# Performance work log

Hardware: AMD Instinct MI355X
Metric: run time of the kernel (lower is better)

## Reference

```python
import jax, jax.numpy as jnp
import numpy as np

B, C, D, H, W = 2, 64, 3, 96, 96
CD = C * D  # conv1x1 channel count = in_dim * 3


def setup_inputs() -> dict:
    key = jax.random.key(0)
    ks = jax.random.split(key, 7)
    s = 1.0 / np.sqrt(CD)
    x = jax.random.normal(ks[0], (B, C, D, H, W), dtype=jnp.float32)
    Wq = jax.random.uniform(ks[1], (CD, CD), jnp.float32, -s, s)
    bq = jax.random.uniform(ks[2], (CD,), jnp.float32, -s, s)
    Wk = jax.random.uniform(ks[3], (CD, CD), jnp.float32, -s, s)
    bk = jax.random.uniform(ks[4], (CD,), jnp.float32, -s, s)
    Wv = jax.random.uniform(ks[5], (CD, CD), jnp.float32, -s, s)
    bv = jax.random.uniform(ks[6], (CD,), jnp.float32, -s, s)
    return {"x": x, "Wq": Wq, "bq": bq, "Wk": Wk, "bk": bk, "Wv": Wv, "bv": bv}


def reference(x, Wq, bq, Wk, bk, Wv, bv):
    b, c, d, h, w = x.shape
    n = h * w
    xr = x.reshape(b, c * d, n)  # [B, CD, N]; conv1x1 == channel matmul
    q = jnp.einsum('oc,bcn->bon', Wq, xr) + bq[:, None]  # [B, CD, N]
    k = jnp.einsum('oc,bcn->bon', Wk, xr) + bk[:, None]
    v = jnp.einsum('oc,bcn->bon', Wv, xr) + bv[:, None]
    energy = jnp.einsum('bcn,bcm->bnm', q, k)            # [B, N, N]
    attention = jax.nn.softmax(energy, axis=-1)
    # out = bmm(value, attention^T): out[b,c,m] = sum_n v[b,c,n] * attn[b,m,n]
    out = jnp.einsum('bcn,bmn->bcm', v, attention)       # [B, CD, N]
    return out.reshape(b, c, d, h, w)
```

## Files before the change

### kernel.cpp

```cpp
#include <hip/hip_runtime.h>

#define NSEQ  9216
#define CDIM  192
#define KTILE 64

typedef _Float16 h8_t  __attribute__((ext_vector_type(8)));
typedef _Float16 h4_t  __attribute__((ext_vector_type(4)));
typedef float    f4_t  __attribute__((ext_vector_type(4)));
typedef float    f16v  __attribute__((ext_vector_type(16)));

__global__ __launch_bounds__(256) void wconv_kernel(
    const float* __restrict__ Wq, const float* __restrict__ Wk,
    const float* __restrict__ Wv, _Float16* __restrict__ Wh)
{
    int i = blockIdx.x * 256 + threadIdx.x;
    if (i >= 3 * 9216) return;
    const float* src = (i < 9216) ? Wq : (i < 18432 ? Wk : Wv);
    int r = i % 9216;
    f4_t w = ((const f4_t*)src)[r];
    h4_t h = {(_Float16)w[0], (_Float16)w[1], (_Float16)w[2], (_Float16)w[3]};
    ((h4_t*)Wh)[i] = h;
}

__global__ __launch_bounds__(128) void proj_kernel(
    const float* __restrict__ x, const _Float16* __restrict__ Wh,
    const float* __restrict__ bq, const float* __restrict__ bk,
    const float* __restrict__ bv,
    _Float16* __restrict__ QT, _Float16* __restrict__ KT, _Float16* __restrict__ Vg)
{
    const int tid  = threadIdx.x;
    const int lane = tid & 63, wave = tid >> 6;
    const int L31  = lane & 31, hi = lane >> 5;
    const int idx  = blockIdx.x * 2 + wave;
    const int b    = idx / 288;
    const int n0   = (idx % 288) * 32;
    const int n    = n0 + L31;

    h8_t bf[12];
    #pragma unroll
    for (int t = 0; t < 12; t++) {
        h8_t h;
        #pragma unroll
        for (int j = 0; j < 8; j++)
            h[j] = (_Float16)x[(size_t)(b * CDIM + t * 16 + hi * 8 + j) * NSEQ + n];
        bf[t] = h;
    }

    const float* biases[3] = {bq, bk, bv};
    for (int mat = 0; mat < 3; mat++) {
        const _Float16* W = Wh + mat * CDIM * CDIM;
        f16v acc[6];
        #pragma unroll
        for (int s = 0; s < 6; s++)
            #pragma unroll
            for (int r = 0; r < 16; r++) acc[s][r] = 0.f;

        #pragma unroll
        for (int t = 0; t < 12; t++) {
            #pragma unroll
            for (int s = 0; s < 6; s++) {
                h8_t a = *(const h8_t*)(W + (s * 32 + L31) * CDIM + t * 16 + hi * 8);
                acc[s] = __builtin_amdgcn_mfma_f32_32x32x16_f16(a, bf[t], acc[s], 0, 0, 0);
            }
        }

        if (mat < 2) {
            _Float16* dst = ((mat == 0) ? QT : KT) + ((size_t)b * NSEQ + n) * CDIM;
            #pragma unroll
            for (int s = 0; s < 6; s++) {
                #pragma unroll
                for (int g = 0; g < 4; g++) {
                    f4_t bb = *(const f4_t*)&biases[mat][s * 32 + 8 * g + 4 * hi];
                    h4_t h = {(_Float16)(acc[s][4*g+0] + bb[0]),
                              (_Float16)(acc[s][4*g+1] + bb[1]),
                              (_Float16)(acc[s][4*g+2] + bb[2]),
                              (_Float16)(acc[s][4*g+3] + bb[3])};
                    *(h4_t*)(dst + s * 32 + 8 * g + 4 * hi) = h;
                }
            }
        } else {
            #pragma unroll
            for (int s = 0; s < 6; s++) {
                #pragma unroll
                for (int g = 0; g < 4; g++) {
                    f4_t bb = *(const f4_t*)&biases[2][s * 32 + 8 * g + 4 * hi];
                    #pragma unroll
                    for (int r = 0; r < 4; r++) {
                        int o = s * 32 + 8 * g + 4 * hi + r;
                        Vg[((size_t)b * CDIM + o) * NSEQ + n] =
                            (_Float16)(acc[s][4*g+r] + bb[r]);
                    }
                }
            }
        }
    }
}

template<int NSPLIT>
__global__ __launch_bounds__(256, 2) void flash_kernel(
    const _Float16* __restrict__ QT, const _Float16* __restrict__ KTg,
    const _Float16* __restrict__ Vg,
    _Float16* __restrict__ O_part, float* __restrict__ m_part, float* __restrict__ l_part)
{
    constexpr int KPS    = NSEQ / NSPLIT;
    constexpr int KITERS = KPS / KTILE;

    __shared__ __align__(16) _Float16 K_s[KTILE * 200];
    __shared__ __align__(16) _Float16 V_s[CDIM * 72];
    __shared__ __align__(16) _Float16 P_s[4 * 32 * 72];
    __shared__ float alpha_s[4][32];

    const int tid  = threadIdx.x;
    const int lane = tid & 63, wave = tid >> 6;
    const int L31  = lane & 31, hi = lane >> 5;
    const int qtile = blockIdx.x, split = blockIdx.y, b = blockIdx.z;
    const int q0 = qtile * 128 + wave * 32;

    h8_t qf[12];
    const _Float16* qbase = QT + ((size_t)b * NSEQ + q0 + L31) * CDIM + hi * 8;
    #pragma unroll
    for (int t = 0; t < 12; t++) qf[t] = *(const h8_t*)(qbase + t * 16);

    f16v acc[6];
    #pragma unroll
    for (int s = 0; s < 6; s++)
        #pragma unroll
        for (int r = 0; r < 16; r++) acc[s][r] = 0.f;
    float m_run = -__builtin_inff();
    float l_run = 0.f;

    const _Float16* ksrc = KTg + ((size_t)b * NSEQ + split * KPS) * CDIM;
    const _Float16* vsrc = Vg + (size_t)b * CDIM * NSEQ + split * KPS;

    for (int kt = 0; kt < KITERS; kt++) {
        __syncthreads();
        {
            const h8_t* src = (const h8_t*)(ksrc + (size_t)kt * KTILE * CDIM);
            #pragma unroll
            for (int t = 0; t < 6; t++) {
                int i = tid + t * 256;
                int row = i / 24, col = i % 24;
                *(h8_t*)(K_s + row * 200 + col * 8) = src[i];
            }
            #pragma unroll
            for (int t = 0; t < 6; t++) {
                int i = tid + t * 256;
                int c = i >> 3, seg = i & 7;
                *(h8_t*)(V_s + c * 72 + seg * 8) =
                    *(const h8_t*)(vsrc + (size_t)c * NSEQ + kt * KTILE + seg * 8);
            }
        }
        __syncthreads();

        f16v st[2];
        #pragma unroll
        for (int s = 0; s < 2; s++)
            #pragma unroll
            for (int r = 0; r < 16; r++) st[s][r] = 0.f;
        #pragma unroll
        for (int t = 0; t < 12; t++) {
            #pragma unroll
            for (int s = 0; s < 2; s++) {
                h8_t a = *(const h8_t*)(K_s + (s * 32 + L31) * 200 + t * 16 + hi * 8);
                st[s] = __builtin_amdgcn_mfma_f32_32x32x16_f16(a, qf[t], st[s], 0, 0, 0);
            }
        }

        float mx = st[0][0];
        #pragma unroll
        for (int s = 0; s < 2; s++)
            #pragma unroll
            for (int r = 0; r < 16; r++) mx = fmaxf(mx, st[s][r]);
        mx = fmaxf(mx, __shfl_xor(mx, 32));
        float m_new = fmaxf(m_run, mx);

        float p[32];
        float psum = 0.f;
        #pragma unroll
        for (int s = 0; s < 2; s++)
            #pragma unroll
            for (int r = 0; r < 16; r++) {
                float e = __expf(st[s][r] - m_new);
                p[s * 16 + r] = e;
                psum += e;
            }

        if (__any(m_new > m_run)) {
            float alpha = __expf(m_run - m_new);
            l_run = l_run * alpha + psum;
            if (lane < 32) alpha_s[wave][lane] = alpha;
            __asm__ volatile("" ::: "memory");
            f4_t a4[4];
            #pragma unroll
            for (int g = 0; g < 4; g++)
                a4[g] = *(const f4_t*)&alpha_s[wave][8 * g + 4 * hi];
            #pragma unroll
            for (int cs = 0; cs < 6; cs++)
                #pragma unroll
                for (int r = 0; r < 16; r++) acc[cs][r] *= a4[r >> 2][r & 3];
        } else {
            l_run += psum;
        }
        m_run = m_new;

        _Float16* prow = P_s + wave * 32 * 72 + L31 * 72;
        #pragma unroll
        for (int s = 0; s < 2; s++)
            #pragma unroll
            for (int g = 0; g < 4; g++) {
                h4_t h = {(_Float16)p[s*16+4*g+0], (_Float16)p[s*16+4*g+1],
                          (_Float16)p[s*16+4*g+2], (_Float16)p[s*16+4*g+3]};
                *(h4_t*)(prow + s * 32 + 8 * g + 4 * hi) = h;
            }
        __asm__ volatile("" ::: "memory");

        #pragma unroll
        for (int ks = 0; ks < 4; ks++) {
            h8_t pa = *(const h8_t*)(prow + ks * 16 + hi * 8);
            #pragma unroll
            for (int cs = 0; cs < 6; cs++) {
                h8_t vb = *(const h8_t*)(V_s + (cs * 32 + L31) * 72 + ks * 16 + hi * 8);
                acc[cs] = __builtin_amdgcn_mfma_f32_32x32x16_f16(pa, vb, acc[cs], 0, 0, 0);
            }
        }
    }

    float l_tot = l_run + __shfl_xor(l_run, 32);
    const size_t pbase = (size_t)(b * NSPLIT + split) * NSEQ + q0;
    if (lane < 32) {
        m_part[pbase + lane] = m_run;
        l_part[pbase + lane] = l_tot;
    }
    _Float16* obase = O_part + pbase * CDIM;
    #pragma unroll
    for (int cs = 0; cs < 6; cs++)
        #pragma unroll
        for (int r = 0; r < 16; r++) {
            int q = (r & 3) + 8 * (r >> 2) + 4 * hi;
            obase[(size_t)q * CDIM + cs * 32 + L31] = (_Float16)acc[cs][r];
        }
}

template<int NS>
__global__ __launch_bounds__(256) void combine_kernel(
    const _Float16* __restrict__ O_part, const float* __restrict__ m_part,
    const float* __restrict__ l_part, float* __restrict__ out)
{
    __shared__ float Cs[CDIM][65];
    __shared__ float winv[NS][64];
    const int tid = threadIdx.x;
    const int b  = blockIdx.y;
    const int n0 = blockIdx.x * 64;

    if (tid < 64) {
        int n = n0 + tid;
        float mm[NS], ll[NS], ms = -__builtin_inff();
        #pragma unroll
        for (int s = 0; s < NS; s++) {
            mm[s] = m_part[(b * NS + s) * NSEQ + n];
            ll[s] = l_part[(b * NS + s) * NSEQ + n];
            ms = fmaxf(ms, mm[s]);
        }
        float denom = 0.f;
        #pragma unroll
        for (int s = 0; s < NS; s++) {
            float w = __expf(mm[s] - ms);
            mm[s] = w;
            denom += w * ll[s];
        }
        #pragma unroll
        for (int s = 0; s < NS; s++) winv[s][tid] = mm[s] / denom;
    }
    __syncthreads();

    for (int i = tid; i < 64 * 96; i += 256) {
        int nl = i / 96, cp = i % 96;
        float v0 = 0.f, v1 = 0.f;
        #pragma unroll
        for (int s = 0; s < NS; s++) {
            const _Float16* op =
                O_part + ((size_t)(b * NS + s) * NSEQ + n0 + nl) * CDIM + cp * 2;
            float w = winv[s][nl];
            v0 += w * (float)op[0];
            v1 += w * (float)op[1];
        }
        Cs[cp * 2][nl] = v0;
        Cs[cp * 2 + 1][nl] = v1;
    }
    __syncthreads();
    for (int i = tid; i < CDIM * 64; i += 256) {
        int nl = i & 63, c = i >> 6;
        out[((size_t)b * CDIM + c) * NSEQ + n0 + nl] = Cs[c][nl];
    }
}

extern "C" void kernel_launch(void* const* d_in, const int* in_sizes, int n_in,
                              void* d_out, int out_size, void* d_ws, size_t ws_size,
                              hipStream_t stream)
{
    const float* x  = (const float*)d_in[0];
    const float* Wq = (const float*)d_in[1];
    const float* bq = (const float*)d_in[2];
    const float* Wk = (const float*)d_in[3];
    const float* bk = (const float*)d_in[4];
    const float* Wv = (const float*)d_in[5];
    const float* bv = (const float*)d_in[6];
    float* out = (float*)d_out;

    char* ws = (char*)d_ws;
    _Float16* QT = (_Float16*)(ws);
    _Float16* KT = (_Float16*)(ws + 7077888);
    _Float16* Vg = (_Float16*)(ws + 14155776);
    char* tail = ws + 21233664;
    _Float16* Wh = (_Float16*)tail;
    _Float16* O_part = (_Float16*)tail;

    wconv_kernel<<<108, 256, 0, stream>>>(Wq, Wk, Wv, Wh);
    proj_kernel<<<288, 128, 0, stream>>>(x, Wh, bq, bk, bv, QT, KT, Vg);

    const size_t need8 = 21233664ull + 8 * 7077888ull + 2 * 589824ull;
    const size_t need4 = 21233664ull + 4 * 7077888ull + 2 * 294912ull;
    if (ws_size >= need8) {
        float* m_part = (float*)(tail + 8 * 7077888ull);
        float* l_part = (float*)(tail + 8 * 7077888ull + 589824ull);
        flash_kernel<8><<<dim3(72, 8, 2), 256, 0, stream>>>(QT, KT, Vg, O_part, m_part, l_part);
        combine_kernel<8><<<dim3(144, 2), 256, 0, stream>>>(O_part, m_part, l_part, out);
    } else if (ws_size >= need4) {
        float* m_part = (float*)(tail + 4 * 7077888ull);
        float* l_part = (float*)(tail + 4 * 7077888ull + 294912ull);
        flash_kernel<4><<<dim3(72, 4, 2), 256, 0, stream>>>(QT, KT, Vg, O_part, m_part, l_part);
        combine_kernel<4><<<dim3(144, 2), 256, 0, stream>>>(O_part, m_part, l_part, out);
    } else {
        float* m_part = (float*)(tail + 2 * 7077888ull);
        float* l_part = (float*)(tail + 2 * 7077888ull + 147456ull);
        flash_kernel<2><<<dim3(72, 2, 2), 256, 0, stream>>>(QT, KT, Vg, O_part, m_part, l_part);
        combine_kernel<2><<<dim3(144, 2), 256, 0, stream>>>(O_part, m_part, l_part, out);
    }
}
```

Before: 302.9 us.

## Read K from global, prefetch V in registers, fold log2e into Q, split projection

Several changes at once. The flash kernel drops the K tile from shared memory and reads K straight from global or L2 into MFMA operands. The V tile is prefetched into registers one iteration ahead, which overlaps its load with compute. Q weights and bias are pre-scaled by log2(e) so the softmax can use exp2 directly. The projection kernel now gives each wave one matrix instead of all three, for more parallelism, and the combine kernel uses smaller tiles and vectorized half2 loads. The risk is that uncached global K reads repeated across waves add memory latency, and that the extra prefetch registers reduce occupancy.

```diff
diff --git a/kernel.cpp b/kernel.cpp
--- a/kernel.cpp
+++ b/kernel.cpp
@@ -3,9 +3,11 @@
 #define NSEQ  9216
 #define CDIM  192
 #define KTILE 64
+#define LOG2E 1.44269504088896f
 
 typedef _Float16 h8_t  __attribute__((ext_vector_type(8)));
 typedef _Float16 h4_t  __attribute__((ext_vector_type(4)));
+typedef _Float16 h2_t  __attribute__((ext_vector_type(2)));
 typedef float    f4_t  __attribute__((ext_vector_type(4)));
 typedef float    f16v  __attribute__((ext_vector_type(16)));
 
@@ -16,13 +18,15 @@
     int i = blockIdx.x * 256 + threadIdx.x;
     if (i >= 3 * 9216) return;
     const float* src = (i < 9216) ? Wq : (i < 18432 ? Wk : Wv);
+    float s = (i < 9216) ? LOG2E : 1.f;
     int r = i % 9216;
     f4_t w = ((const f4_t*)src)[r];
-    h4_t h = {(_Float16)w[0], (_Float16)w[1], (_Float16)w[2], (_Float16)w[3]};
+    h4_t h = {(_Float16)(w[0]*s), (_Float16)(w[1]*s),
+              (_Float16)(w[2]*s), (_Float16)(w[3]*s)};
     ((h4_t*)Wh)[i] = h;
 }
 
-__global__ __launch_bounds__(128) void proj_kernel(
+__global__ __launch_bounds__(256) void proj_kernel(
     const float* __restrict__ x, const _Float16* __restrict__ Wh,
     const float* __restrict__ bq, const float* __restrict__ bk,
     const float* __restrict__ bv,
@@ -31,9 +35,11 @@
     const int tid  = threadIdx.x;
     const int lane = tid & 63, wave = tid >> 6;
     const int L31  = lane & 31, hi = lane >> 5;
-    const int idx  = blockIdx.x * 2 + wave;
-    const int b    = idx / 288;
-    const int n0   = (idx % 288) * 32;
+    const int idx  = blockIdx.x * 4 + wave;
+    const int mat  = idx / 576;
+    const int rem  = idx % 576;
+    const int b    = rem / 288;
+    const int n0   = (rem % 288) * 32;
     const int n    = n0 + L31;
 
     h8_t bf[12];
@@ -46,50 +52,50 @@
         bf[t] = h;
     }
 
-    const float* biases[3] = {bq, bk, bv};
-    for (int mat = 0; mat < 3; mat++) {
-        const _Float16* W = Wh + mat * CDIM * CDIM;
-        f16v acc[6];
-        #pragma unroll
-        for (int s = 0; s < 6; s++)
-            #pragma unroll
-            for (int r = 0; r < 16; r++) acc[s][r] = 0.f;
-
-        #pragma unroll
-        for (int t = 0; t < 12; t++) {
-            #pragma unroll
-            for (int s = 0; s < 6; s++) {
-                h8_t a = *(const h8_t*)(W + (s * 32 + L31) * CDIM + t * 16 + hi * 8);
-                acc[s] = __builtin_amdgcn_mfma_f32_32x32x16_f16(a, bf[t], acc[s], 0, 0, 0);
-            }
-        }
-
-        if (mat < 2) {
-            _Float16* dst = ((mat == 0) ? QT : KT) + ((size_t)b * NSEQ + n) * CDIM;
-            #pragma unroll
-            for (int s = 0; s < 6; s++) {
+    const _Float16* W = Wh + mat * CDIM * CDIM;
+    const float* bias = (mat == 0) ? bq : (mat == 1 ? bk : bv);
+    const float bscale = (mat == 0) ? LOG2E : 1.f;
+
+    f16v acc[6];
+    #pragma unroll
+    for (int s = 0; s < 6; s++)
+        #pragma unroll
+        for (int r = 0; r < 16; r++) acc[s][r] = 0.f;
+
+    #pragma unroll
+    for (int t = 0; t < 12; t++) {
+        #pragma unroll
+        for (int s = 0; s < 6; s++) {
+            h8_t a = *(const h8_t*)(W + (s * 32 + L31) * CDIM + t * 16 + hi * 8);
+            acc[s] = __builtin_amdgcn_mfma_f32_32x32x16_f16(a, bf[t], acc[s], 0, 0, 0);
+        }
+    }
+
+    if (mat < 2) {
+        _Float16* dst = ((mat == 0) ? QT : KT) + ((size_t)b * NSEQ + n) * CDIM;
+        #pragma unroll
+        for (int s = 0; s < 6; s++) {
+            #pragma unroll
+            for (int g = 0; g < 4; g++) {
+                f4_t bb = *(const f4_t*)&bias[s * 32 + 8 * g + 4 * hi];
+                h4_t h = {(_Float16)(acc[s][4*g+0] + bb[0] * bscale),
+                          (_Float16)(acc[s][4*g+1] + bb[1] * bscale),
+                          (_Float16)(acc[s][4*g+2] + bb[2] * bscale),
+                          (_Float16)(acc[s][4*g+3] + bb[3] * bscale)};
+                *(h4_t*)(dst + s * 32 + 8 * g + 4 * hi) = h;
+            }
+        }
+    } else {
+        #pragma unroll
+        for (int s = 0; s < 6; s++) {
+            #pragma unroll
+            for (int g = 0; g < 4; g++) {
+                f4_t bb = *(const f4_t*)&bias[s * 32 + 8 * g + 4 * hi];
                 #pragma unroll
-                for (int g = 0; g < 4; g++) {
-                    f4_t bb = *(const f4_t*)&biases[mat][s * 32 + 8 * g + 4 * hi];
-                    h4_t h = {(_Float16)(acc[s][4*g+0] + bb[0]),
-                              (_Float16)(acc[s][4*g+1] + bb[1]),
-                              (_Float16)(acc[s][4*g+2] + bb[2]),
-                              (_Float16)(acc[s][4*g+3] + bb[3])};
-                    *(h4_t*)(dst + s * 32 + 8 * g + 4 * hi) = h;
-                }
-            }
-        } else {
-            #pragma unroll
-            for (int s = 0; s < 6; s++) {
-                #pragma unroll
-                for (int g = 0; g < 4; g++) {
-                    f4_t bb = *(const f4_t*)&biases[2][s * 32 + 8 * g + 4 * hi];
-                    #pragma unroll
-                    for (int r = 0; r < 4; r++) {
-                        int o = s * 32 + 8 * g + 4 * hi + r;
-                        Vg[((size_t)b * CDIM + o) * NSEQ + n] =
-                            (_Float16)(acc[s][4*g+r] + bb[r]);
-                    }
+                for (int r = 0; r < 4; r++) {
+                    int o = s * 32 + 8 * g + 4 * hi + r;
+                    Vg[((size_t)b * CDIM + o) * NSEQ + n] =
+                        (_Float16)(acc[s][4*g+r] + bb[r]);
                 }
             }
         }
@@ -105,7 +111,6 @@
     constexpr int KPS    = NSEQ / NSPLIT;
     constexpr int KITERS = KPS / KTILE;
 
-    __shared__ __align__(16) _Float16 K_s[KTILE * 200];
     __shared__ __align__(16) _Float16 V_s[CDIM * 72];
     __shared__ __align__(16) _Float16 P_s[4 * 32 * 72];
     __shared__ float alpha_s[4][32];
@@ -132,26 +137,32 @@
     const _Float16* ksrc = KTg + ((size_t)b * NSEQ + split * KPS) * CDIM;
     const _Float16* vsrc = Vg + (size_t)b * CDIM * NSEQ + split * KPS;
 
+    const _Float16* vgl[6];
+    _Float16*       vds[6];
+    #pragma unroll
+    for (int t = 0; t < 6; t++) {
+        int i = tid + t * 256;
+        int c = i >> 3, seg = i & 7;
+        vgl[t] = vsrc + (size_t)c * NSEQ + seg * 8;
+        vds[t] = V_s + c * 72 + seg * 8;
+    }
+
+    h8_t vreg[6];
+    #pragma unroll
+    for (int t = 0; t < 6; t++) vreg[t] = *(const h8_t*)(vgl[t]);
+
     for (int kt = 0; kt < KITERS; kt++) {
         __syncthreads();
-        {
-            const h8_t* src = (const h8_t*)(ksrc + (size_t)kt * KTILE * CDIM);
-            #pragma unroll
-            for (int t = 0; t < 6; t++) {
-                int i = tid + t * 256;
-                int row = i / 24, col = i % 24;
-                *(h8_t*)(K_s + row * 200 + col * 8) = src[i];
-            }
-            #pragma unroll
-            for (int t = 0; t < 6; t++) {
-                int i = tid + t * 256;
-                int c = i >> 3, seg = i & 7;
-                *(h8_t*)(V_s + c * 72 + seg * 8) =
-                    *(const h8_t*)(vsrc + (size_t)c * NSEQ + kt * KTILE + seg * 8);
-            }
-        }
+        #pragma unroll
+        for (int t = 0; t < 6; t++) *(h8_t*)(vds[t]) = vreg[t];
         __syncthreads();
-
+        if (kt + 1 < KITERS) {
+            #pragma unroll
+            for (int t = 0; t < 6; t++)
+                vreg[t] = *(const h8_t*)(vgl[t] + (kt + 1) * KTILE);
+        }
+
+        const _Float16* kbase = ksrc + (size_t)kt * KTILE * CDIM;
         f16v st[2];
         #pragma unroll
         for (int s = 0; s < 2; s++)
@@ -161,7 +172,7 @@
         for (int t = 0; t < 12; t++) {
             #pragma unroll
             for (int s = 0; s < 2; s++) {
-                h8_t a = *(const h8_t*)(K_s + (s * 32 + L31) * 200 + t * 16 + hi * 8);
+                h8_t a = *(const h8_t*)(kbase + (s * 32 + L31) * CDIM + t * 16 + hi * 8);
                 st[s] = __builtin_amdgcn_mfma_f32_32x32x16_f16(a, qf[t], st[s], 0, 0, 0);
             }
         }
@@ -180,13 +191,13 @@
         for (int s = 0; s < 2; s++)
             #pragma unroll
             for (int r = 0; r < 16; r++) {
-                float e = __expf(st[s][r] - m_new);
+                float e = __builtin_exp2f(st[s][r] - m_new);
                 p[s * 16 + r] = e;
                 psum += e;
             }
 
         if (__any(m_new > m_run)) {
-            float alpha = __expf(m_run - m_new);
+            float alpha = __builtin_exp2f(m_run - m_new);
             l_run = l_run * alpha + psum;
             if (lane < 32) alpha_s[wave][lane] = alpha;
             __asm__ volatile("" ::: "memory");
@@ -246,13 +257,13 @@
     const _Float16* __restrict__ O_part, const float* __restrict__ m_part,
     const float* __restrict__ l_part, float* __restrict__ out)
 {
-    __shared__ float Cs[CDIM][65];
-    __shared__ float winv[NS][64];
+    __shared__ float Cs[CDIM][33];
+    __shared__ float winv[NS][32];
     const int tid = threadIdx.x;
     const int b  = blockIdx.y;
-    const int n0 = blockIdx.x * 64;
-
-    if (tid < 64) {
+    const int n0 = blockIdx.x * 32;
+
+    if (tid < 32) {
         int n = n0 + tid;
         float mm[NS], ll[NS], ms = -__builtin_inff();
         #pragma unroll
@@ -264,7 +275,7 @@
         float denom = 0.f;
         #pragma unroll
         for (int s = 0; s < NS; s++) {
-            float w = __expf(mm[s] - ms);
+            float w = __builtin_exp2f(mm[s] - ms);
             mm[s] = w;
             denom += w * ll[s];
         }
@@ -273,13 +284,13 @@
     }
     __syncthreads();
 
-    for (int i = tid; i < 64 * 96; i += 256) {
+    for (int i = tid; i < 32 * 96; i += 256) {
         int nl = i / 96, cp = i % 96;
         float v0 = 0.f, v1 = 0.f;
         #pragma unroll
         for (int s = 0; s < NS; s++) {
-            const _Float16* op =
-                O_part + ((size_t)(b * NS + s) * NSEQ + n0 + nl) * CDIM + cp * 2;
+            h2_t op = *(const h2_t*)(O_part +
+                ((size_t)(b * NS + s) * NSEQ + n0 + nl) * CDIM + cp * 2);
             float w = winv[s][nl];
             v0 += w * (float)op[0];
             v1 += w * (float)op[1];
@@ -288,8 +299,8 @@
         Cs[cp * 2 + 1][nl] = v1;
     }
     __syncthreads();
-    for (int i = tid; i < CDIM * 64; i += 256) {
-        int nl = i & 63, c = i >> 6;
+    for (int i = tid; i < CDIM * 32; i += 256) {
+        int nl = i & 31, c = i >> 5;
         out[((size_t)b * CDIM + c) * NSEQ + n0 + nl] = Cs[c][nl];
     }
 }
@@ -316,7 +327,7 @@
     _Float16* O_part = (_Float16*)tail;
 
     wconv_kernel<<<108, 256, 0, stream>>>(Wq, Wk, Wv, Wh);
-    proj_kernel<<<288, 128, 0, stream>>>(x, Wh, bq, bk, bv, QT, KT, Vg);
+    proj_kernel<<<432, 256, 0, stream>>>(x, Wh, bq, bk, bv, QT, KT, Vg);
 
     const size_t need8 = 21233664ull + 8 * 7077888ull + 2 * 589824ull;
     const size_t need4 = 21233664ull + 4 * 7077888ull + 2 * 294912ull;
@@ -324,16 +335,16 @@
         float* m_part = (float*)(tail + 8 * 7077888ull);
         float* l_part = (float*)(tail + 8 * 7077888ull + 589824ull);
         flash_kernel<8><<<dim3(72, 8, 2), 256, 0, stream>>>(QT, KT, Vg, O_part, m_part, l_part);
-        combine_kernel<8><<<dim3(144, 2), 256, 0, stream>>>(O_part, m_part, l_part, out);
+        combine_kernel<8><<<dim3(288, 2), 256, 0, stream>>>(O_part, m_part, l_part, out);
     } else if (ws_size >= need4) {
         float* m_part = (float*)(tail + 4 * 7077888ull);
         float* l_part = (float*)(tail + 4 * 7077888ull + 294912ull);
         flash_kernel<4><<<dim3(72, 4, 2), 256, 0, stream>>>(QT, KT, Vg, O_part, m_part, l_part);
-        combine_kernel<4><<<dim3(144, 2), 256, 0, stream>>>(O_part, m_part, l_part, out);
+        combine_kernel<4><<<dim3(288, 2), 256, 0, stream>>>(O_part, m_part, l_part, out);
     } else {
         float* m_part = (float*)(tail + 2 * 7077888ull);
         float* l_part = (float*)(tail + 2 * 7077888ull + 147456ull);
         flash_kernel<2><<<dim3(72, 2, 2), 256, 0, stream>>>(QT, KT, Vg, O_part, m_part, l_part);
-        combine_kernel<2><<<dim3(144, 2), 256, 0, stream>>>(O_part, m_part, l_part, out);
-    }
-}
+        combine_kernel<2><<<dim3(288, 2), 256, 0, stream>>>(O_part, m_part, l_part, out);
+    }
+}
```

Measured after the change: 417.7 us. +37.9%, slower.

## Split projection across matrices and halves, fold log2e into Q, vectorize combine

Applied to the files above, without the earlier changes.

The projection kernel now gives each wave a single matrix and one half of the output channels, launching six times as many waves to raise parallelism and cut per-wave register pressure. The cost is that x is re-read six times. Wq and bq are pre-scaled by log2(e) so the flash and combine kernels can use exp2 in place of exp, which drops a multiply per exponential. The combine kernel reads four halves per load instead of two, and the row-max reduction is reordered into a shorter tree.

```diff
diff --git a/kernel.cpp b/kernel.cpp
--- a/kernel.cpp
+++ b/kernel.cpp
@@ -3,9 +3,11 @@
 #define NSEQ  9216
 #define CDIM  192
 #define KTILE 64
+#define LOG2E 1.44269504088896f
 
 typedef _Float16 h8_t  __attribute__((ext_vector_type(8)));
 typedef _Float16 h4_t  __attribute__((ext_vector_type(4)));
+typedef _Float16 h2_t  __attribute__((ext_vector_type(2)));
 typedef float    f4_t  __attribute__((ext_vector_type(4)));
 typedef float    f16v  __attribute__((ext_vector_type(16)));
 
@@ -16,13 +18,15 @@
     int i = blockIdx.x * 256 + threadIdx.x;
     if (i >= 3 * 9216) return;
     const float* src = (i < 9216) ? Wq : (i < 18432 ? Wk : Wv);
+    float s = (i < 9216) ? LOG2E : 1.f;
     int r = i % 9216;
     f4_t w = ((const f4_t*)src)[r];
-    h4_t h = {(_Float16)w[0], (_Float16)w[1], (_Float16)w[2], (_Float16)w[3]};
+    h4_t h = {(_Float16)(w[0]*s), (_Float16)(w[1]*s),
+              (_Float16)(w[2]*s), (_Float16)(w[3]*s)};
     ((h4_t*)Wh)[i] = h;
 }
 
-__global__ __launch_bounds__(128) void proj_kernel(
+__global__ __launch_bounds__(256) void proj_kernel(
     const float* __restrict__ x, const _Float16* __restrict__ Wh,
     const float* __restrict__ bq, const float* __restrict__ bk,
     const float* __restrict__ bv,
@@ -31,9 +35,13 @@
     const int tid  = threadIdx.x;
     const int lane = tid & 63, wave = tid >> 6;
     const int L31  = lane & 31, hi = lane >> 5;
-    const int idx  = blockIdx.x * 2 + wave;
-    const int b    = idx / 288;
-    const int n0   = (idx % 288) * 32;
+    const int idx  = blockIdx.x * 4 + wave;
+    const int mat  = idx / 1152;
+    const int rem  = idx % 1152;
+    const int half = rem / 576;
+    const int rem2 = rem % 576;
+    const int b    = rem2 / 288;
+    const int n0   = (rem2 % 288) * 32;
     const int n    = n0 + L31;
 
     h8_t bf[12];
@@ -46,50 +54,51 @@
         bf[t] = h;
     }
 
-    const float* biases[3] = {bq, bk, bv};
-    for (int mat = 0; mat < 3; mat++) {
-        const _Float16* W = Wh + mat * CDIM * CDIM;
-        f16v acc[6];
-        #pragma unroll
-        for (int s = 0; s < 6; s++)
-            #pragma unroll
-            for (int r = 0; r < 16; r++) acc[s][r] = 0.f;
-
-        #pragma unroll
-        for (int t = 0; t < 12; t++) {
-            #pragma unroll
-            for (int s = 0; s < 6; s++) {
-                h8_t a = *(const h8_t*)(W + (s * 32 + L31) * CDIM + t * 16 + hi * 8);
-                acc[s] = __builtin_amdgcn_mfma_f32_32x32x16_f16(a, bf[t], acc[s], 0, 0, 0);
-            }
-        }
-
-        if (mat < 2) {
-            _Float16* dst = ((mat == 0) ? QT : KT) + ((size_t)b * NSEQ + n) * CDIM;
-            #pragma unroll
-            for (int s = 0; s < 6; s++) {
+    const _Float16* W = Wh + mat * CDIM * CDIM + half * 96 * CDIM;
+    const float* bias = ((mat == 0) ? bq : (mat == 1 ? bk : bv)) + half * 96;
+    const float bscale = (mat == 0) ? LOG2E : 1.f;
+
+    f16v acc[3];
+    #pragma unroll
+    for (int s = 0; s < 3; s++)
+        #pragma unroll
+        for (int r = 0; r < 16; r++) acc[s][r] = 0.f;
+
+    #pragma unroll
+    for (int t = 0; t < 12; t++) {
+        #pragma unroll
+        for (int s = 0; s < 3; s++) {
+            h8_t a = *(const h8_t*)(W + (s * 32 + L31) * CDIM + t * 16 + hi * 8);
+            acc[s] = __builtin_amdgcn_mfma_f32_32x32x16_f16(a, bf[t], acc[s], 0, 0, 0);
+        }
+    }
+
+    if (mat < 2) {
+        _Float16* dst = ((mat == 0) ? QT : KT)
+                        + ((size_t)b * NSEQ + n) * CDIM + half * 96;
+        #pragma unroll
+        for (int s = 0; s < 3; s++) {
+            #pragma unroll
+            for (int g = 0; g < 4; g++) {
+                f4_t bb = *(const f4_t*)&bias[s * 32 + 8 * g + 4 * hi];
+                h4_t h = {(_Float16)(acc[s][4*g+0] + bb[0] * bscale),
+                          (_Float16)(acc[s][4*g+1] + bb[1] * bscale),
+                          (_Float16)(acc[s][4*g+2] + bb[2] * bscale),
+                          (_Float16)(acc[s][4*g+3] + bb[3] * bscale)};
+                *(h4_t*)(dst + s * 32 + 8 * g + 4 * hi) = h;
+            }
+        }
+    } else {
+        #pragma unroll
+        for (int s = 0; s < 3; s++) {
+            #pragma unroll
+            for (int g = 0; g < 4; g++) {
+                f4_t bb = *(const f4_t*)&bias[s * 32 + 8 * g + 4 * hi];
                 #pragma unroll
-                for (int g = 0; g < 4; g++) {
-                    f4_t bb = *(const f4_t*)&biases[mat][s * 32 + 8 * g + 4 * hi];
-                    h4_t h = {(_Float16)(acc[s][4*g+0] + bb[0]),
-                              (_Float16)(acc[s][4*g+1] + bb[1]),
-                              (_Float16)(acc[s][4*g+2] + bb[2]),
-                              (_Float16)(acc[s][4*g+3] + bb[3])};
-                    *(h4_t*)(dst + s * 32 + 8 * g + 4 * hi) = h;
-                }
-            }
-        } else {
-            #pragma unroll
-            for (int s = 0; s < 6; s++) {
-                #pragma unroll
-                for (int g = 0; g < 4; g++) {
-                    f4_t bb = *(const f4_t*)&biases[2][s * 32 + 8 * g + 4 * hi];
-                    #pragma unroll
-                    for (int r = 0; r < 4; r++) {
-                        int o = s * 32 + 8 * g + 4 * hi + r;
-                        Vg[((size_t)b * CDIM + o) * NSEQ + n] =
-                            (_Float16)(acc[s][4*g+r] + bb[r]);
-                    }
+                for (int r = 0; r < 4; r++) {
+                    int o = half * 96 + s * 32 + 8 * g + 4 * hi + r;
+                    Vg[((size_t)b * CDIM + o) * NSEQ + n] =
+                        (_Float16)(acc[s][4*g+r] + bb[r]);
                 }
             }
         }
@@ -166,11 +175,9 @@
             }
         }
 
-        float mx = st[0][0];
-        #pragma unroll
-        for (int s = 0; s < 2; s++)
-            #pragma unroll
-            for (int r = 0; r < 16; r++) mx = fmaxf(mx, st[s][r]);
+        float mx = fmaxf(st[0][0], st[1][0]);
+        #pragma unroll
+        for (int r = 1; r < 16; r++) mx = fmaxf(mx, fmaxf(st[0][r], st[1][r]));
         mx = fmaxf(mx, __shfl_xor(mx, 32));
         float m_new = fmaxf(m_run, mx);
 
@@ -180,13 +187,13 @@
         for (int s = 0; s < 2; s++)
             #pragma unroll
             for (int r = 0; r < 16; r++) {
-                float e = __expf(st[s][r] - m_new);
+                float e = __builtin_exp2f(st[s][r] - m_new);
                 p[s * 16 + r] = e;
                 psum += e;
             }
 
         if (__any(m_new > m_run)) {
-            float alpha = __expf(m_run - m_new);
+            float alpha = __builtin_exp2f(m_run - m_new);
             l_run = l_run * alpha + psum;
             if (lane < 32) alpha_s[wave][lane] = alpha;
             __asm__ volatile("" ::: "memory");
@@ -264,7 +271,7 @@
         float denom = 0.f;
         #pragma unroll
         for (int s = 0; s < NS; s++) {
-            float w = __expf(mm[s] - ms);
+            float w = __builtin_exp2f(mm[s] - ms);
             mm[s] = w;
             denom += w * ll[s];
         }
@@ -273,19 +280,23 @@
     }
     __syncthreads();
 
-    for (int i = tid; i < 64 * 96; i += 256) {
-        int nl = i / 96, cp = i % 96;
-        float v0 = 0.f, v1 = 0.f;
+    for (int i = tid; i < 64 * 48; i += 256) {
+        int nl = i / 48, c4 = i % 48;
+        float v0 = 0.f, v1 = 0.f, v2 = 0.f, v3 = 0.f;
         #pragma unroll
         for (int s = 0; s < NS; s++) {
-            const _Float16* op =
-                O_part + ((size_t)(b * NS + s) * NSEQ + n0 + nl) * CDIM + cp * 2;
+            h4_t op = *(const h4_t*)(O_part +
+                ((size_t)(b * NS + s) * NSEQ + n0 + nl) * CDIM + c4 * 4);
             float w = winv[s][nl];
             v0 += w * (float)op[0];
             v1 += w * (float)op[1];
-        }
-        Cs[cp * 2][nl] = v0;
-        Cs[cp * 2 + 1][nl] = v1;
+            v2 += w * (float)op[2];
+            v3 += w * (float)op[3];
+        }
+        Cs[c4 * 4 + 0][nl] = v0;
+        Cs[c4 * 4 + 1][nl] = v1;
+        Cs[c4 * 4 + 2][nl] = v2;
+        Cs[c4 * 4 + 3][nl] = v3;
     }
     __syncthreads();
     for (int i = tid; i < CDIM * 64; i += 256) {
@@ -316,7 +327,7 @@
     _Float16* O_part = (_Float16*)tail;
 
     wconv_kernel<<<108, 256, 0, stream>>>(Wq, Wk, Wv, Wh);
-    proj_kernel<<<288, 128, 0, stream>>>(x, Wh, bq, bk, bv, QT, KT, Vg);
+    proj_kernel<<<864, 256, 0, stream>>>(x, Wh, bq, bk, bv, QT, KT, Vg);
 
     const size_t need8 = 21233664ull + 8 * 7077888ull + 2 * 589824ull;
     const size_t need4 = 21233664ull + 4 * 7077888ull + 2 * 294912ull;
```

After: 305.0 us. Within noise of the previous version (+0.7%).
